# Kernel tuning notes

Hardware: AMD Instinct MI355X
Metric: run time of the kernel (lower is better)

The kernel has to match this reference:

```python
import jax, jax.numpy as jnp
import numpy as np

# Balanced binary-tree tensorized circuit (CP sum-product layers), cirkit-style.
B, D, C, K, NCLS = 256, 256, 1, 256, 10
LEVELS = 8  # log2(D); each level halves the number of regions


def setup_inputs() -> dict:
    key = jax.random.key(0)
    ks = jax.random.split(key, LEVELS + 3)
    inp = {"x": jax.random.normal(ks[0], (B, D, C), dtype=jnp.float32)}
    # Input layer params: per-variable linear map C -> K units
    inp["W_in"] = jax.random.normal(ks[1], (D, C, K), dtype=jnp.float32)
    # CP layer params per tree level: (n_regions, arity=2, K_in, K_out)
    n = D
    for l in range(LEVELS):
        n //= 2
        inp[f"W_lvl{l}"] = jax.random.normal(ks[2 + l], (n, 2, K, K), dtype=jnp.float32)
    # Output mixing layer K -> num_classes
    inp["W_out"] = jax.random.normal(ks[2 + LEVELS], (K, NCLS), dtype=jnp.float32)
    return inp


def _circuit(x, W_in, W_lvls, W_out):
    # Input layers: gather scope (here: each var is its own scope) + per-var map.
    # (B, D, C) x (D, C, K) -> (B, D, K); tanh keeps units bounded in [-1, 1].
    h = jnp.tanh(jnp.einsum('bdc,dck->bdk', x, W_in))
    # Fused sum-product (CP) layers, one batched einsum per tree level instead of
    # a Python loop over individual small layers.
    for W in W_lvls:
        n = W.shape[0]
        hp = h.reshape(h.shape[0], n, 2, K)          # pair adjacent regions
        Wn = jax.nn.softmax(W, axis=2)               # reparam: convex sum over K_in
        proj = jnp.einsum('bnak,nakj->bnaj', hp, Wn) # per-child sum layer
        h = proj[:, :, 0, :] * proj[:, :, 1, :]      # Hadamard product layer
    root = h[:, 0, :]                                # (B, K)
    out = jnp.einsum('bk,kc->bc', root, jax.nn.softmax(W_out, axis=0))
    return out[:, None, :]                           # (B, num_out=1, num_cls)


def reference(x, W_in, W_lvl0, W_lvl1, W_lvl2, W_lvl3, W_lvl4, W_lvl5, W_lvl6, W_lvl7, W_out):
    W_lvls = [W_lvl0, W_lvl1, W_lvl2, W_lvl3, W_lvl4, W_lvl5, W_lvl6, W_lvl7]
    return _circuit(x, W_in, W_lvls, W_out)
```

## Files before the change

### kernel.cpp

```cpp
#include <hip/hip_runtime.h>

#define NCLS 10

typedef __attribute__((ext_vector_type(8))) short short8;
typedef __attribute__((ext_vector_type(4))) float f32x4;

__device__ __forceinline__ float bf2f(ushort u) {
    return __uint_as_float(((unsigned int)u) << 16);
}
__device__ __forceinline__ ushort f2bf(float f) {
    unsigned int u = __float_as_uint(f);
    u = (u + 0x7FFFu + ((u >> 16) & 1u)) >> 16;
    return (ushort)u;
}
__device__ __forceinline__ float tanh_fast(float v) {
    float t = __expf(2.f * v);
    return (t - 1.f) / (t + 1.f);
}
__device__ __forceinline__ void gll16(const void* g, void* s) {
    __builtin_amdgcn_global_load_lds(
        (const __attribute__((address_space(1))) void*)g,
        (__attribute__((address_space(3))) void*)s, 16, 0, 0);
}

__device__ void exp_tile(const float* __restrict__ Wb, ushort* __restrict__ Eb,
                         float* __restrict__ rcp_row, const int j0)
{
    __shared__ float sT[64][68];
    __shared__ float sC[4][64];
    const int tid = threadIdx.x;
    const int lj = tid & 63;
    const int kq = tid >> 6;
    const int jj = (tid & 15) * 4;
    const int kk = tid >> 4;
    float csum = 0.f;

    for (int kb = 0; kb < 4; ++kb) {
        #pragma unroll
        for (int p = 0; p < 4; ++p) {
            const int k = kb * 64 + p * 16 + kk;
            *(float4*)&sT[p * 16 + kk][jj] = *(const float4*)&Wb[(size_t)k * 256 + j0 + jj];
        }
        __syncthreads();
        ushort pk[16];
        #pragma unroll
        for (int t = 0; t < 16; ++t) {
            const float e = __expf(sT[kq * 16 + t][lj]);
            csum += e;
            pk[t] = f2bf(e);
        }
        short8 v0, v1;
        #pragma unroll
        for (int e2 = 0; e2 < 8; ++e2) { v0[e2] = (short)pk[e2]; v1[e2] = (short)pk[8 + e2]; }
        ushort* dst = Eb + (size_t)(j0 + lj) * 256 + kb * 64 + kq * 16;
        *(short8*)dst = v0;
        *(short8*)(dst + 8) = v1;
        __syncthreads();
    }
    sC[kq][lj] = csum;
    __syncthreads();
    if (tid < 64)
        rcp_row[j0 + tid] = 1.f / (sC[0][tid] + sC[1][tid] + sC[2][tid] + sC[3][tid]);
}

__global__ __launch_bounds__(256)
void prep1_kernel(const float* __restrict__ W0, const float* __restrict__ x,
                  const float* __restrict__ Win, ushort* __restrict__ E0,
                  float* __restrict__ Rcp0, ushort* __restrict__ H0)
{
    const int bid = blockIdx.x;
    if (bid < 1024) {
        const int ia = bid >> 2, jt = bid & 3;
        exp_tile(W0 + (size_t)ia * 65536, E0 + ((size_t)ia << 16),
                 Rcp0 + (size_t)ia * 256, jt * 64);
    } else {
        __shared__ float sX[256];
        const int d = bid - 1024;
        const int tid = threadIdx.x;
        sX[tid] = x[(size_t)tid * 256 + d];
        __syncthreads();
        const int k2 = (tid & 127) * 2;
        const int boff = tid >> 7;
        const float2 wv = *(const float2*)&Win[(size_t)d * 256 + k2];
        for (int b2 = 0; b2 < 256; b2 += 2) {
            const int b = b2 + boff;
            const float xb = sX[b];
            const unsigned int u0 = f2bf(tanh_fast(xb * wv.x));
            const unsigned int u1 = f2bf(tanh_fast(xb * wv.y));
            *(unsigned int*)&H0[((size_t)b * 256 + d) * 256 + k2] = u0 | (u1 << 16);
        }
    }
}

__global__ __launch_bounds__(256)
void exp0_kernel(const float* __restrict__ W, ushort* __restrict__ E,
                 float* __restrict__ Rcp)
{
    const int ia = blockIdx.y;
    const int j0 = blockIdx.x * 64;
    exp_tile(W + (size_t)ia * 65536, E + ((size_t)ia << 16),
             Rcp + (size_t)ia * 256, j0);
}

__global__ __launch_bounds__(256)
void prep2_kernel(const float* __restrict__ W1, const float* __restrict__ W2,
                  const float* __restrict__ W3, const float* __restrict__ W4,
                  const float* __restrict__ W5, const float* __restrict__ W6,
                  const float* __restrict__ W7,
                  ushort* __restrict__ Ebase, float* __restrict__ RcpBase)
{
    int rem = blockIdx.x;
    int lvl = 1, n2 = 128;
    while (rem >= n2 * 4 && lvl < 7) { rem -= n2 * 4; n2 >>= 1; ++lvl; }
    const int jt = rem & 3;
    const int ia = rem >> 2;
    const float* W;
    switch (lvl) {
        case 1: W = W1; break; case 2: W = W2; break; case 3: W = W3; break;
        case 4: W = W4; break; case 5: W = W5; break; case 6: W = W6; break;
        default: W = W7; break;
    }
    size_t eoff = 0; int rrow = 256;
    for (int m = 1; m < lvl; ++m) { eoff += ((size_t)(256 >> m)) << 16; rrow += (256 >> m); }
    exp_tile(W + (size_t)ia * 65536,
             Ebase + eoff + ((size_t)ia << 16),
             RcpBase + (size_t)(rrow + ia) * 256, jt * 64);
}

template<int BM, int WR, int WC, int LB, bool TANH>
__global__ __launch_bounds__(256, LB)
void level_kernel(const float* __restrict__ x, const float* __restrict__ Win,
                  const ushort* __restrict__ H, const ushort* __restrict__ E,
                  const float* __restrict__ Rcp, ushort* __restrict__ Hout,
                  const int n, const int lg)
{
    constexpr int MF = BM / (16 * WR);
    constexpr int NF = 64 / (16 * WC);
    constexpr int NBH = 256 / BM;
    constexpr int AUNITS = 2 * BM / 16;
    constexpr int UITER = (AUNITS + 3) / 4;

    __shared__ __align__(16) char sA[2][2][BM * 64];
    __shared__ __align__(16) char sB[2][2][64 * 64];

    const int tid = threadIdx.x;
    const int bid = blockIdx.x;
    const int i   = bid & (n - 1);
    const int s   = bid >> lg;
    const int bh  = s % NBH;
    const int jt  = s / NBH;
    const int b0  = bh * BM;
    const int j0  = jt * 64;
    const int np  = 2 * n;

    const int l   = tid & 63;
    const int l15 = l & 15;
    const int g   = l >> 4;
    const int w   = tid >> 6;
    const int wm  = w / WC;
    const int wn  = w % WC;

    f32x4 acc[2][MF][NF];
    #pragma unroll
    for (int a2 = 0; a2 < 2; ++a2)
        #pragma unroll
        for (int mf = 0; mf < MF; ++mf)
            #pragma unroll
            for (int nf = 0; nf < NF; ++nf)
                acc[a2][mf][nf] = (f32x4){0.f, 0.f, 0.f, 0.f};

    float xv = 0.f;
    int ta = 0, trow = 0;
    if (TANH) {
        ta = tid >> 7; trow = tid & 127;
        xv = x[(size_t)(b0 + trow) * 256 + 2 * i + ta];
    }

    auto stage = [&](int buf, int k0) {
        if constexpr (TANH) {
            const float* wrow = &Win[(size_t)(2 * i + ta) * 256 + k0];
            char* base = &sA[ta][buf][trow * 64];
            const int sr = (trow >> 1) & 3;
            #pragma unroll
            for (int c = 0; c < 4; ++c) {
                const float4 w0 = *(const float4*)&wrow[c * 8];
                const float4 w1 = *(const float4*)&wrow[c * 8 + 4];
                short8 v;
                v[0] = (short)f2bf(tanh_fast(xv * w0.x));
                v[1] = (short)f2bf(tanh_fast(xv * w0.y));
                v[2] = (short)f2bf(tanh_fast(xv * w0.z));
                v[3] = (short)f2bf(tanh_fast(xv * w0.w));
                v[4] = (short)f2bf(tanh_fast(xv * w1.x));
                v[5] = (short)f2bf(tanh_fast(xv * w1.y));
                v[6] = (short)f2bf(tanh_fast(xv * w1.z));
                v[7] = (short)f2bf(tanh_fast(xv * w1.w));
                *(short8*)(base + ((c ^ sr) << 4)) = v;
            }
        } else {
            #pragma unroll
            for (int uu = 0; uu < UITER; ++uu) {
                const int u = w + uu * 4;
                if (u < AUNITS) {
                    const int ua  = u / (BM / 16);
                    const int r16 = (u % (BM / 16)) * 16;
                    const int row = r16 + (l >> 2);
                    const int c   = l & 3;
                    const ushort* src = H
                        + ((size_t)(b0 + row) * np + (2 * i + ua)) * 256
                        + k0 + ((c ^ ((row >> 1) & 3)) << 3);
                    gll16(src, &sA[ua][buf][r16 * 64]);
                }
            }
        }
        #pragma unroll
        for (int vv = 0; vv < 2; ++vv) {
            const int v    = w + vv * 4;
            const int ea   = v >> 2;
            const int jr16 = (v & 3) * 16;
            const int jr   = jr16 + (l >> 2);
            const int c    = l & 3;
            const ushort* src = E + ((size_t)(2 * i + ea) << 16)
                + (size_t)(j0 + jr) * 256
                + k0 + ((c ^ ((jr >> 1) & 3)) << 3);
            gll16(src, &sB[ea][buf][jr16 * 64]);
        }
    };

    stage(0, 0);
    __syncthreads();

    for (int t = 0; t < 8; ++t) {
        const int buf = t & 1;
        if (t < 7) stage(buf ^ 1, (t + 1) * 32);

        short8 afr[2][MF];
        short8 bfr[2][NF];
        #pragma unroll
        for (int a2 = 0; a2 < 2; ++a2) {
            #pragma unroll
            for (int nf = 0; nf < NF; ++nf) {
                const int jr = wn * (NF * 16) + nf * 16 + l15;
                bfr[a2][nf] = *(const short8*)&sB[a2][buf][jr * 64 + ((g ^ ((jr >> 1) & 3)) << 4)];
            }
            #pragma unroll
            for (int mf = 0; mf < MF; ++mf) {
                const int row = wm * (MF * 16) + mf * 16 + l15;
                afr[a2][mf] = *(const short8*)&sA[a2][buf][row * 64 + ((g ^ ((row >> 1) & 3)) << 4)];
            }
        }
        #pragma unroll
        for (int a2 = 0; a2 < 2; ++a2)
            #pragma unroll
            for (int mf = 0; mf < MF; ++mf)
                #pragma unroll
                for (int nf = 0; nf < NF; ++nf)
                    acc[a2][mf][nf] = __builtin_amdgcn_mfma_f32_16x16x32_bf16(
                        afr[a2][mf], bfr[a2][nf], acc[a2][mf][nf], 0, 0, 0);
        __syncthreads();
    }

    float rc[2][NF];
    #pragma unroll
    for (int a2 = 0; a2 < 2; ++a2)
        #pragma unroll
        for (int nf = 0; nf < NF; ++nf)
            rc[a2][nf] = Rcp[(size_t)(2 * i + a2) * 256 + j0 + wn * (NF * 16) + nf * 16 + l15];

    #pragma unroll
    for (int mf = 0; mf < MF; ++mf)
        #pragma unroll
        for (int nf = 0; nf < NF; ++nf) {
            const int j = j0 + wn * (NF * 16) + nf * 16 + l15;
            #pragma unroll
            for (int r = 0; r < 4; ++r) {
                const int b = b0 + wm * (MF * 16) + mf * 16 + g * 4 + r;
                const float v0 = acc[0][mf][nf][r] * rc[0][nf];
                const float v1 = acc[1][mf][nf][r] * rc[1][nf];
                Hout[((size_t)b * n + i) * 256 + j] = f2bf(v0 * v1);
            }
        }
}

__global__ __launch_bounds__(256)
void out_kernel(const ushort* __restrict__ root, const float* __restrict__ Wout,
                float* __restrict__ out)
{
    __shared__ float sR[16][260];
    __shared__ float sE2[256][12];
    __shared__ float sDen[16];
    const int tid = threadIdx.x;
    if (tid < 16) sDen[tid] = 0.f;
    __syncthreads();
    float e[NCLS];
    #pragma unroll
    for (int c = 0; c < NCLS; ++c) {
        e[c] = __expf(Wout[(size_t)tid * NCLS + c]);
        sE2[tid][c] = e[c];
    }
    #pragma unroll
    for (int c = 0; c < NCLS; ++c) {
        float v = e[c];
        for (int off = 32; off > 0; off >>= 1) v += __shfl_down(v, off);
        if ((tid & 63) == 0) atomicAdd(&sDen[c], v);
    }
    const int b0 = blockIdx.x * 16;
    #pragma unroll
    for (int v = 0; v < 4; ++v) {
        const int u = v * 256 + tid;
        const int row = u >> 6;
        const int c4 = (u & 63) * 4;
        const ushort4 p = *(const ushort4*)&root[(size_t)(b0 + row) * 256 + c4];
        sR[row][c4 + 0] = bf2f(p.x);
        sR[row][c4 + 1] = bf2f(p.y);
        sR[row][c4 + 2] = bf2f(p.z);
        sR[row][c4 + 3] = bf2f(p.w);
    }
    __syncthreads();
    const int ty = tid >> 4, tx = tid & 15;
    if (tx < NCLS) {
        float s = 0.f;
        for (int k = 0; k < 256; ++k) s += sR[ty][k] * sE2[k][tx];
        out[(size_t)(b0 + ty) * NCLS + tx] = s / sDen[tx];
    }
}

extern "C" void kernel_launch(void* const* d_in, const int* in_sizes, int n_in,
                              void* d_out, int out_size, void* d_ws, size_t ws_size,
                              hipStream_t stream)
{
    const float* x    = (const float*)d_in[0];
    const float* Win  = (const float*)d_in[1];
    const float* Wl[8];
    for (int lv = 0; lv < 8; ++lv) Wl[lv] = (const float*)d_in[2 + lv];
    const float* Wout = (const float*)d_in[10];
    float* out = (float*)d_out;

    char* wsb = (char*)d_ws;
    static const size_t ecum[8] = {0, 0, 128, 192, 224, 240, 248, 252};

    if (ws_size >= 84408320ull) {
        ushort* A0 = (ushort*)wsb;
        ushort* A1 = (ushort*)(wsb + 16777216);
        ushort* C  = (ushort*)(wsb + 33554432);
        ushort* B  = (ushort*)(wsb + 50331648);
        float*  RC = (float*)(wsb + 83886080);

        prep1_kernel<<<dim3(1280), 256, 0, stream>>>(Wl[0], x, Win, A0, RC, B);
        level_kernel<128, 2, 2, 3, false><<<dim3(8 * 128), 256, 0, stream>>>(
            nullptr, nullptr, B, A0, RC, C, 128, 7);
        prep2_kernel<<<dim3(1016), 256, 0, stream>>>(
            Wl[1], Wl[2], Wl[3], Wl[4], Wl[5], Wl[6], Wl[7], B, RC);

        level_kernel<64, 2, 2, 4, false><<<dim3(16 * 64), 256, 0, stream>>>(
            nullptr, nullptr, C, B + (ecum[1] << 16), RC + (256 + ecum[1]) * 256, A0, 64, 6);
        level_kernel<64, 2, 2, 4, false><<<dim3(16 * 32), 256, 0, stream>>>(
            nullptr, nullptr, A0, B + (ecum[2] << 16), RC + (256 + ecum[2]) * 256, A1, 32, 5);
        level_kernel<32, 2, 2, 4, false><<<dim3(32 * 16), 256, 0, stream>>>(
            nullptr, nullptr, A1, B + (ecum[3] << 16), RC + (256 + ecum[3]) * 256, A0, 16, 4);
        level_kernel<32, 2, 2, 4, false><<<dim3(32 * 8), 256, 0, stream>>>(
            nullptr, nullptr, A0, B + (ecum[4] << 16), RC + (256 + ecum[4]) * 256, A1, 8, 3);
        level_kernel<16, 1, 4, 4, false><<<dim3(64 * 4), 256, 0, stream>>>(
            nullptr, nullptr, A1, B + (ecum[5] << 16), RC + (256 + ecum[5]) * 256, A0, 4, 2);
        level_kernel<16, 1, 4, 4, false><<<dim3(64 * 2), 256, 0, stream>>>(
            nullptr, nullptr, A0, B + (ecum[6] << 16), RC + (256 + ecum[6]) * 256, A1, 2, 1);
        level_kernel<16, 1, 4, 4, false><<<dim3(64 * 1), 256, 0, stream>>>(
            nullptr, nullptr, A1, B + (ecum[7] << 16), RC + (256 + ecum[7]) * 256, A0, 1, 0);
        out_kernel<<<dim3(16), 256, 0, stream>>>(A0, Wout, out);
    } else {
        ushort* R1 = (ushort*)wsb;
        ushort* R2 = (ushort*)(wsb + 33554432);
        ushort* R3 = (ushort*)(wsb + 50331648);
        float*  RC = (float*)(wsb + 58720256);

        exp0_kernel<<<dim3(4, 256), 256, 0, stream>>>(Wl[0], R1, RC);
        level_kernel<128, 2, 2, 3, true><<<dim3(8 * 128), 256, 0, stream>>>(
            x, Win, nullptr, R1, RC, R2, 128, 7);
        prep2_kernel<<<dim3(1016), 256, 0, stream>>>(
            Wl[1], Wl[2], Wl[3], Wl[4], Wl[5], Wl[6], Wl[7], R1, RC);

        level_kernel<64, 2, 2, 4, false><<<dim3(16 * 64), 256, 0, stream>>>(
            nullptr, nullptr, R2, R1 + (ecum[1] << 16), RC + (256 + ecum[1]) * 256, R3, 64, 6);
        level_kernel<64, 2, 2, 4, false><<<dim3(16 * 32), 256, 0, stream>>>(
            nullptr, nullptr, R3, R1 + (ecum[2] << 16), RC + (256 + ecum[2]) * 256, R2, 32, 5);
        level_kernel<32, 2, 2, 4, false><<<dim3(32 * 16), 256, 0, stream>>>(
            nullptr, nullptr, R2, R1 + (ecum[3] << 16), RC + (256 + ecum[3]) * 256, R3, 16, 4);
        level_kernel<32, 2, 2, 4, false><<<dim3(32 * 8), 256, 0, stream>>>(
            nullptr, nullptr, R3, R1 + (ecum[4] << 16), RC + (256 + ecum[4]) * 256, R2, 8, 3);
        level_kernel<16, 1, 4, 4, false><<<dim3(64 * 4), 256, 0, stream>>>(
            nullptr, nullptr, R2, R1 + (ecum[5] << 16), RC + (256 + ecum[5]) * 256, R3, 4, 2);
        level_kernel<16, 1, 4, 4, false><<<dim3(64 * 2), 256, 0, stream>>>(
            nullptr, nullptr, R3, R1 + (ecum[6] << 16), RC + (256 + ecum[6]) * 256, R2, 2, 1);
        level_kernel<16, 1, 4, 4, false><<<dim3(64 * 1), 256, 0, stream>>>(
            nullptr, nullptr, R2, R1 + (ecum[7] << 16), RC + (256 + ecum[7]) * 256, R3, 1, 0);
        out_kernel<<<dim3(16), 256, 0, stream>>>(R3, Wout, out);
    }
}
```

Baseline: 272.9 us.

## Fuse last three levels and output into one tail kernel; restructure exp and input prep

```diff
diff --git a/kernel.cpp b/kernel.cpp
--- a/kernel.cpp
+++ b/kernel.cpp
@@ -26,33 +26,43 @@
 __device__ void exp_tile(const float* __restrict__ Wb, ushort* __restrict__ Eb,
                          float* __restrict__ rcp_row, const int j0)
 {
-    __shared__ float sT[64][68];
+    __shared__ ushort sT[2][64][72];
     __shared__ float sC[4][64];
     const int tid = threadIdx.x;
-    const int lj = tid & 63;
-    const int kq = tid >> 6;
+    const int kk = tid >> 4;
     const int jj = (tid & 15) * 4;
-    const int kk = tid >> 4;
+    const int lj = tid >> 2;
+    const int kq = tid & 3;
     float csum = 0.f;
 
-    for (int kb = 0; kb < 4; ++kb) {
+    auto load = [&](int buf, int c) {
         #pragma unroll
         for (int p = 0; p < 4; ++p) {
-            const int k = kb * 64 + p * 16 + kk;
-            *(float4*)&sT[p * 16 + kk][jj] = *(const float4*)&Wb[(size_t)k * 256 + j0 + jj];
-        }
-        __syncthreads();
+            const int row = p * 16 + kk;
+            const float4 wv = *(const float4*)&Wb[(size_t)(c * 64 + row) * 256 + j0 + jj];
+            ushort4 o;
+            o.x = f2bf(__expf(wv.x)); o.y = f2bf(__expf(wv.y));
+            o.z = f2bf(__expf(wv.z)); o.w = f2bf(__expf(wv.w));
+            *(ushort4*)&sT[buf][row][jj] = o;
+        }
+    };
+
+    load(0, 0);
+    __syncthreads();
+    for (int c = 0; c < 4; ++c) {
+        const int buf = c & 1;
+        if (c < 3) load(buf ^ 1, c + 1);
         ushort pk[16];
         #pragma unroll
         for (int t = 0; t < 16; ++t) {
-            const float e = __expf(sT[kq * 16 + t][lj]);
-            csum += e;
-            pk[t] = f2bf(e);
+            const ushort u = sT[buf][kq * 16 + t][lj];
+            pk[t] = u;
+            csum += bf2f(u);
         }
         short8 v0, v1;
         #pragma unroll
         for (int e2 = 0; e2 < 8; ++e2) { v0[e2] = (short)pk[e2]; v1[e2] = (short)pk[8 + e2]; }
-        ushort* dst = Eb + (size_t)(j0 + lj) * 256 + kb * 64 + kq * 16;
+        ushort* dst = Eb + (size_t)(j0 + lj) * 256 + c * 64 + kq * 16;
         *(short8*)dst = v0;
         *(short8*)(dst + 8) = v1;
         __syncthreads();
@@ -74,32 +84,24 @@
         exp_tile(W0 + (size_t)ia * 65536, E0 + ((size_t)ia << 16),
                  Rcp0 + (size_t)ia * 256, jt * 64);
     } else {
-        __shared__ float sX[256];
-        const int d = bid - 1024;
+        __shared__ float sXr[256];
+        const int hb = bid - 1024;
+        const int b  = hb >> 1;
+        const int kh = (hb & 1) * 128;
         const int tid = threadIdx.x;
-        sX[tid] = x[(size_t)tid * 256 + d];
+        sXr[tid] = x[(size_t)b * 256 + tid];
         __syncthreads();
-        const int k2 = (tid & 127) * 2;
-        const int boff = tid >> 7;
-        const float2 wv = *(const float2*)&Win[(size_t)d * 256 + k2];
-        for (int b2 = 0; b2 < 256; b2 += 2) {
-            const int b = b2 + boff;
-            const float xb = sX[b];
+        const int k  = kh + (tid & 63) * 2;
+        const int dw = tid >> 6;
+        for (int d0 = 0; d0 < 256; d0 += 4) {
+            const int d = d0 + dw;
+            const float2 wv = *(const float2*)&Win[(size_t)d * 256 + k];
+            const float xb = sXr[d];
             const unsigned int u0 = f2bf(tanh_fast(xb * wv.x));
             const unsigned int u1 = f2bf(tanh_fast(xb * wv.y));
-            *(unsigned int*)&H0[((size_t)b * 256 + d) * 256 + k2] = u0 | (u1 << 16);
-        }
-    }
-}
-
-__global__ __launch_bounds__(256)
-void exp0_kernel(const float* __restrict__ W, ushort* __restrict__ E,
-                 float* __restrict__ Rcp)
-{
-    const int ia = blockIdx.y;
-    const int j0 = blockIdx.x * 64;
-    exp_tile(W + (size_t)ia * 65536, E + ((size_t)ia << 16),
-             Rcp + (size_t)ia * 256, j0);
+            *(unsigned int*)&H0[((size_t)b * 256 + d) * 256 + k] = u0 | (u1 << 16);
+        }
+    }
 }
 
 __global__ __launch_bounds__(256)
@@ -127,10 +129,9 @@
              RcpBase + (size_t)(rrow + ia) * 256, jt * 64);
 }
 
-template<int BM, int WR, int WC, int LB, bool TANH>
+template<int BM, int WR, int WC, int LB>
 __global__ __launch_bounds__(256, LB)
-void level_kernel(const float* __restrict__ x, const float* __restrict__ Win,
-                  const ushort* __restrict__ H, const ushort* __restrict__ E,
+void level_kernel(const ushort* __restrict__ H, const ushort* __restrict__ E,
                   const float* __restrict__ Rcp, ushort* __restrict__ Hout,
                   const int n, const int lg)
 {
@@ -169,47 +170,19 @@
             for (int nf = 0; nf < NF; ++nf)
                 acc[a2][mf][nf] = (f32x4){0.f, 0.f, 0.f, 0.f};
 
-    float xv = 0.f;
-    int ta = 0, trow = 0;
-    if (TANH) {
-        ta = tid >> 7; trow = tid & 127;
-        xv = x[(size_t)(b0 + trow) * 256 + 2 * i + ta];
-    }
-
     auto stage = [&](int buf, int k0) {
-        if constexpr (TANH) {
-            const float* wrow = &Win[(size_t)(2 * i + ta) * 256 + k0];
-            char* base = &sA[ta][buf][trow * 64];
-            const int sr = (trow >> 1) & 3;
-            #pragma unroll
-            for (int c = 0; c < 4; ++c) {
-                const float4 w0 = *(const float4*)&wrow[c * 8];
-                const float4 w1 = *(const float4*)&wrow[c * 8 + 4];
-                short8 v;
-                v[0] = (short)f2bf(tanh_fast(xv * w0.x));
-                v[1] = (short)f2bf(tanh_fast(xv * w0.y));
-                v[2] = (short)f2bf(tanh_fast(xv * w0.z));
-                v[3] = (short)f2bf(tanh_fast(xv * w0.w));
-                v[4] = (short)f2bf(tanh_fast(xv * w1.x));
-                v[5] = (short)f2bf(tanh_fast(xv * w1.y));
-                v[6] = (short)f2bf(tanh_fast(xv * w1.z));
-                v[7] = (short)f2bf(tanh_fast(xv * w1.w));
-                *(short8*)(base + ((c ^ sr) << 4)) = v;
-            }
-        } else {
-            #pragma unroll
-            for (int uu = 0; uu < UITER; ++uu) {
-                const int u = w + uu * 4;
-                if (u < AUNITS) {
-                    const int ua  = u / (BM / 16);
-                    const int r16 = (u % (BM / 16)) * 16;
-                    const int row = r16 + (l >> 2);
-                    const int c   = l & 3;
-                    const ushort* src = H
-                        + ((size_t)(b0 + row) * np + (2 * i + ua)) * 256
-                        + k0 + ((c ^ ((row >> 1) & 3)) << 3);
-                    gll16(src, &sA[ua][buf][r16 * 64]);
-                }
+        #pragma unroll
+        for (int uu = 0; uu < UITER; ++uu) {
+            const int u = w + uu * 4;
+            if (u < AUNITS) {
+                const int ua  = u / (BM / 16);
+                const int r16 = (u % (BM / 16)) * 16;
+                const int row = r16 + (l >> 2);
+                const int c   = l & 3;
+                const ushort* src = H
+                    + ((size_t)(b0 + row) * np + (2 * i + ua)) * 256
+                    + k0 + ((c ^ ((row >> 1) & 3)) << 3);
+                gll16(src, &sA[ua][buf][r16 * 64]);
             }
         }
         #pragma unroll
@@ -281,45 +254,105 @@
         }
 }
 
-__global__ __launch_bounds__(256)
-void out_kernel(const ushort* __restrict__ root, const float* __restrict__ Wout,
-                float* __restrict__ out)
-{
-    __shared__ float sR[16][260];
-    __shared__ float sE2[256][12];
+__global__ __launch_bounds__(256, 1)
+void tail_kernel(const ushort* __restrict__ H5,
+                 const ushort* __restrict__ E5, const ushort* __restrict__ E6,
+                 const ushort* __restrict__ E7,
+                 const float* __restrict__ R5, const float* __restrict__ R6,
+                 const float* __restrict__ R7,
+                 const float* __restrict__ Wout, float* __restrict__ out)
+{
+    __shared__ __align__(16) ushort sP[16 * 2048];
+    __shared__ __align__(16) ushort sQ[16 * 1024];
+    __shared__ float sEW[256][12];
     __shared__ float sDen[16];
+
     const int tid = threadIdx.x;
+    const int b0  = blockIdx.x * 16;
+    const int l   = tid & 63;
+    const int l15 = l & 15;
+    const int g   = l >> 4;
+    const int w   = tid >> 6;
+
     if (tid < 16) sDen[tid] = 0.f;
-    __syncthreads();
+
+    for (int it = 0; it < 16; ++it) {
+        const ushort* src = H5 + (size_t)(b0 + it) * 2048 + ((tid ^ (it & 7)) << 3);
+        gll16(src, &sP[it * 2048 + w * 512]);
+    }
+
     float e[NCLS];
     #pragma unroll
     for (int c = 0; c < NCLS; ++c) {
         e[c] = __expf(Wout[(size_t)tid * NCLS + c]);
-        sE2[tid][c] = e[c];
-    }
+        sEW[tid][c] = e[c];
+    }
+    __syncthreads();
     #pragma unroll
     for (int c = 0; c < NCLS; ++c) {
         float v = e[c];
         for (int off = 32; off > 0; off >>= 1) v += __shfl_down(v, off);
         if ((tid & 63) == 0) atomicAdd(&sDen[c], v);
     }
-    const int b0 = blockIdx.x * 16;
-    #pragma unroll
-    for (int v = 0; v < 4; ++v) {
-        const int u = v * 256 + tid;
-        const int row = u >> 6;
-        const int c4 = (u & 63) * 4;
-        const ushort4 p = *(const ushort4*)&root[(size_t)(b0 + row) * 256 + c4];
-        sR[row][c4 + 0] = bf2f(p.x);
-        sR[row][c4 + 1] = bf2f(p.y);
-        sR[row][c4 + 2] = bf2f(p.z);
-        sR[row][c4 + 3] = bf2f(p.w);
-    }
-    __syncthreads();
+
+    auto level = [&](const ushort* src, int np_in, ushort* dst,
+                     const ushort* El, const float* Rl) {
+        const int pairs  = np_in >> 1;
+        const int rl_in  = np_in * 256;
+        const int rl_out = pairs * 256;
+        const int j0w    = w * 64;
+        for (int i = 0; i < pairs; ++i) {
+            f32x4 acc[2][4];
+            #pragma unroll
+            for (int a = 0; a < 2; ++a)
+                #pragma unroll
+                for (int nf = 0; nf < 4; ++nf) acc[a][nf] = (f32x4){0.f,0.f,0.f,0.f};
+            for (int t = 0; t < 8; ++t) {
+                #pragma unroll
+                for (int a = 0; a < 2; ++a) {
+                    const int kidx = (2 * i + a) * 256 + t * 32 + g * 8;
+                    const int slot = kidx >> 3;
+                    const short8 afr = *(const short8*)&src[l15 * rl_in + ((slot ^ (l15 & 7)) << 3)];
+                    #pragma unroll
+                    for (int nf = 0; nf < 4; ++nf) {
+                        const int j = j0w + nf * 16 + l15;
+                        const short8 bfr = *(const short8*)&El[((size_t)(2 * i + a) << 16)
+                                                               + (size_t)j * 256 + t * 32 + g * 8];
+                        acc[a][nf] = __builtin_amdgcn_mfma_f32_16x16x32_bf16(
+                            afr, bfr, acc[a][nf], 0, 0, 0);
+                    }
+                }
+            }
+            #pragma unroll
+            for (int nf = 0; nf < 4; ++nf) {
+                const int j = j0w + nf * 16 + l15;
+                const float r0 = Rl[(2 * i + 0) * 256 + j];
+                const float r1 = Rl[(2 * i + 1) * 256 + j];
+                #pragma unroll
+                for (int r = 0; r < 4; ++r) {
+                    const int row  = g * 4 + r;
+                    const float v  = (acc[0][nf][r] * r0) * (acc[1][nf][r] * r1);
+                    const int oidx = i * 256 + j;
+                    const int oslot = oidx >> 3;
+                    dst[row * rl_out + ((oslot ^ (row & 7)) << 3) + (oidx & 7)] = f2bf(v);
+                }
+            }
+        }
+        __syncthreads();
+    };
+
+    level(sP, 8, sQ, E5, R5);
+    level(sQ, 4, sP, E6, R6);
+    level(sP, 2, sQ, E7, R7);
+
     const int ty = tid >> 4, tx = tid & 15;
     if (tx < NCLS) {
         float s = 0.f;
-        for (int k = 0; k < 256; ++k) s += sR[ty][k] * sE2[k][tx];
+        for (int k = 0; k < 256; ++k) {
+            const int slot = k >> 3;
+            const ushort u = sQ[ty * 256 + ((slot ^ (ty & 7)) << 3) + (k & 7)];
+            s += bf2f(u) * sEW[k][tx];
+        }
         out[(size_t)(b0 + ty) * NCLS + tx] = s / sDen[tx];
     }
 }
@@ -336,62 +369,33 @@
     float* out = (float*)d_out;
 
     char* wsb = (char*)d_ws;
+    ushort* A0 = (ushort*)wsb;
+    ushort* A1 = (ushort*)(wsb + 16777216);
+    ushort* C  = (ushort*)(wsb + 33554432);
+    ushort* B  = (ushort*)(wsb + 50331648);
+    float*  RC = (float*)(wsb + 83886080);
+
     static const size_t ecum[8] = {0, 0, 128, 192, 224, 240, 248, 252};
 
-    if (ws_size >= 84408320ull) {
-        ushort* A0 = (ushort*)wsb;
-        ushort* A1 = (ushort*)(wsb + 16777216);
-        ushort* C  = (ushort*)(wsb + 33554432);
-        ushort* B  = (ushort*)(wsb + 50331648);
-        float*  RC = (float*)(wsb + 83886080);
-
-        prep1_kernel<<<dim3(1280), 256, 0, stream>>>(Wl[0], x, Win, A0, RC, B);
-        level_kernel<128, 2, 2, 3, false><<<dim3(8 * 128), 256, 0, stream>>>(
-            nullptr, nullptr, B, A0, RC, C, 128, 7);
-        prep2_kernel<<<dim3(1016), 256, 0, stream>>>(
-            Wl[1], Wl[2], Wl[3], Wl[4], Wl[5], Wl[6], Wl[7], B, RC);
-
-        level_kernel<64, 2, 2, 4, false><<<dim3(16 * 64), 256, 0, stream>>>(
-            nullptr, nullptr, C, B + (ecum[1] << 16), RC + (256 + ecum[1]) * 256, A0, 64, 6);
-        level_kernel<64, 2, 2, 4, false><<<dim3(16 * 32), 256, 0, stream>>>(
-            nullptr, nullptr, A0, B + (ecum[2] << 16), RC + (256 + ecum[2]) * 256, A1, 32, 5);
-        level_kernel<32, 2, 2, 4, false><<<dim3(32 * 16), 256, 0, stream>>>(
-            nullptr, nullptr, A1, B + (ecum[3] << 16), RC + (256 + ecum[3]) * 256, A0, 16, 4);
-        level_kernel<32, 2, 2, 4, false><<<dim3(32 * 8), 256, 0, stream>>>(
-            nullptr, nullptr, A0, B + (ecum[4] << 16), RC + (256 + ecum[4]) * 256, A1, 8, 3);
-        level_kernel<16, 1, 4, 4, false><<<dim3(64 * 4), 256, 0, stream>>>(
-            nullptr, nullptr, A1, B + (ecum[5] << 16), RC + (256 + ecum[5]) * 256, A0, 4, 2);
-        level_kernel<16, 1, 4, 4, false><<<dim3(64 * 2), 256, 0, stream>>>(
-            nullptr, nullptr, A0, B + (ecum[6] << 16), RC + (256 + ecum[6]) * 256, A1, 2, 1);
-        level_kernel<16, 1, 4, 4, false><<<dim3(64 * 1), 256, 0, stream>>>(
-            nullptr, nullptr, A1, B + (ecum[7] << 16), RC + (256 + ecum[7]) * 256, A0, 1, 0);
-        out_kernel<<<dim3(16), 256, 0, stream>>>(A0, Wout, out);
-    } else {
-        ushort* R1 = (ushort*)wsb;
-        ushort* R2 = (ushort*)(wsb + 33554432);
-        ushort* R3 = (ushort*)(wsb + 50331648);
-        float*  RC = (float*)(wsb + 58720256);
-
-        exp0_kernel<<<dim3(4, 256), 256, 0, stream>>>(Wl[0], R1, RC);
-        level_kernel<128, 2, 2, 3, true><<<dim3(8 * 128), 256, 0, stream>>>(
-            x, Win, nullptr, R1, RC, R2, 128, 7);
-        prep2_kernel<<<dim3(1016), 256, 0, stream>>>(
-            Wl[1], Wl[2], Wl[3], Wl[4], Wl[5], Wl[6], Wl[7], R1, RC);
-
-        level_kernel<64, 2, 2, 4, false><<<dim3(16 * 64), 256, 0, stream>>>(
-            nullptr, nullptr, R2, R1 + (ecum[1] << 16), RC + (256 + ecum[1]) * 256, R3, 64, 6);
-        level_kernel<64, 2, 2, 4, false><<<dim3(16 * 32), 256, 0, stream>>>(
-            nullptr, nullptr, R3, R1 + (ecum[2] << 16), RC + (256 + ecum[2]) * 256, R2, 32, 5);
-        level_kernel<32, 2, 2, 4, false><<<dim3(32 * 16), 256, 0, stream>>>(
-            nullptr, nullptr, R2, R1 + (ecum[3] << 16), RC + (256 + ecum[3]) * 256, R3, 16, 4);
-        level_kernel<32, 2, 2, 4, false><<<dim3(32 * 8), 256, 0, stream>>>(
-            nullptr, nullptr, R3, R1 + (ecum[4] << 16), RC + (256 + ecum[4]) * 256, R2, 8, 3);
-        level_kernel<16, 1, 4, 4, false><<<dim3(64 * 4), 256, 0, stream>>>(
-            nullptr, nullptr, R2, R1 + (ecum[5] << 16), RC + (256 + ecum[5]) * 256, R3, 4, 2);
-        level_kernel<16, 1, 4, 4, false><<<dim3(64 * 2), 256, 0, stream>>>(
-            nullptr, nullptr, R3, R1 + (ecum[6] << 16), RC + (256 + ecum[6]) * 256, R2, 2, 1);
-        level_kernel<16, 1, 4, 4, false><<<dim3(64 * 1), 256, 0, stream>>>(
-            nullptr, nullptr, R2, R1 + (ecum[7] << 16), RC + (256 + ecum[7]) * 256, R3, 1, 0);
-        out_kernel<<<dim3(16), 256, 0, stream>>>(R3, Wout, out);
-    }
-}
+    prep1_kernel<<<dim3(1536), 256, 0, stream>>>(Wl[0], x, Win, A0, RC, B);
+    level_kernel<128, 2, 2, 3><<<dim3(8 * 128), 256, 0, stream>>>(
+        B, A0, RC, C, 128, 7);
+    prep2_kernel<<<dim3(1016), 256, 0, stream>>>(
+        Wl[1], Wl[2], Wl[3], Wl[4], Wl[5], Wl[6], Wl[7], B, RC);
+
+    level_kernel<64, 2, 2, 4><<<dim3(16 * 64), 256, 0, stream>>>(
+        C, B + (ecum[1] << 16), RC + (256 + ecum[1]) * 256, A0, 64, 6);
+    level_kernel<64, 2, 2, 4><<<dim3(16 * 32), 256, 0, stream>>>(
+        A0, B + (ecum[2] << 16), RC + (256 + ecum[2]) * 256, A1, 32, 5);
+    level_kernel<32, 2, 2, 4><<<dim3(32 * 16), 256, 0, stream>>>(
+        A1, B + (ecum[3] << 16), RC + (256 + ecum[3]) * 256, A0, 16, 4);
+    level_kernel<32, 2, 2, 4><<<dim3(32 * 8), 256, 0, stream>>>(
+        A0, B + (ecum[4] << 16), RC + (256 + ecum[4]) * 256, A1, 8, 3);
+
+    tail_kernel<<<dim3(16), 256, 0, stream>>>(
+        A1,
+        B + (ecum[5] << 16), B + (ecum[6] << 16), B + (ecum[7] << 16),
+        RC + (256 + ecum[5]) * 256, RC + (256 + ecum[6]) * 256,
+        RC + (256 + ecum[7]) * 256,
+        Wout, out);
+}
```

Measured after the change: 326.6 us. 19.7% more time.
